# Optimization experiments

Measured on AMD Instinct MI355X. Metric: run time of the kernel, lower is better.

Reference implementation:

```python
import jax, jax.numpy as jnp
import numpy as np

NUM_HEADS = 8
NUM_LEVELS = 4
NUM_POINTS = 16
NUM_BEV = 2
EMBED = 256
BS = 64
NQ = NUM_LEVELS * NUM_POINTS  # 64


def _bilinear_sample(img, grid):
    """F.grid_sample(mode='bilinear', padding_mode='zeros', align_corners=False).
    img: (N, C, H, W); grid: (N, Hg, Wg, 2) in [-1, 1] (x, y). Returns (N, C, Hg, Wg)."""
    N, C, H, W = img.shape
    gx = (grid[..., 0] + 1.0) * (W * 0.5) - 0.5  # (N, Hg, Wg)
    gy = (grid[..., 1] + 1.0) * (H * 0.5) - 0.5
    x0 = jnp.floor(gx)
    y0 = jnp.floor(gy)
    flat = img.reshape(N, C, H * W)

    def gather(xi, yi):
        valid = (xi >= 0) & (xi <= W - 1) & (yi >= 0) & (yi <= H - 1)
        xc = jnp.clip(xi, 0, W - 1).astype(jnp.int32)
        yc = jnp.clip(yi, 0, H - 1).astype(jnp.int32)
        idx = (yc * W + xc).reshape(N, 1, -1)
        g = jnp.take_along_axis(flat, idx, axis=2).reshape(N, C, xi.shape[1], xi.shape[2])
        return g * valid[:, None, :, :].astype(img.dtype)

    wx1 = (gx - x0)[:, None]  # (N,1,Hg,Wg)
    wy1 = (gy - y0)[:, None]
    v00 = gather(x0, y0)
    v01 = gather(x0 + 1.0, y0)
    v10 = gather(x0, y0 + 1.0)
    v11 = gather(x0 + 1.0, y0 + 1.0)
    top = v00 * (1.0 - wx1) + v01 * wx1
    bot = v10 * (1.0 - wx1) + v11 * wx1
    return top * (1.0 - wy1) + bot * wy1


def _forward(query, key_hist, value_hist, reference_points, W_off, b_off, spatial_shapes):
    bs, nq, d = query.shape
    Hn, L, P, BEV = NUM_HEADS, NUM_LEVELS, NUM_POINTS, NUM_BEV
    dh = d // Hn
    Pb = P * BEV
    ss = np.asarray(spatial_shapes)  # (L, 2) static (h, w)

    queries = jnp.concatenate([query, query], axis=1)           # (bs, 2*nq, d)
    keies = jnp.concatenate([query, key_hist], axis=1)
    values = jnp.concatenate([query, value_hist], axis=1)
    qb = queries.shape[1]

    # sampling offsets projection (the only used learned linear in the original forward)
    off = (queries @ W_off + b_off).reshape(bs, qb, Hn, Pb, L, 2)

    # NOTE: original re-assigns q/k/v from the RAW concatenated tensors (to_Q/to_K/to_V discarded)
    qh = queries.reshape(bs, qb, Hn, dh)
    kh = keies.reshape(bs, qb, Hn, dh)
    vh = values.reshape(bs, qb, Hn, dh)

    attn = jax.nn.softmax(jnp.einsum('bqhd,bkhd->bqhk', qh, kh), axis=-1)
    attn = attn.reshape(bs, qb, Hn, L, Pb)

    rp = jnp.concatenate([reference_points, reference_points], axis=1)  # (bs, qb, L, 2)
    norm = jnp.stack([jnp.asarray(ss[:, 1], jnp.float32),
                      jnp.asarray(ss[:, 0], jnp.float32)], axis=-1)      # (L, 2) = (w, h)
    loc = rp[:, :, None, None, :, :] + off / norm                        # (bs,qb,H,Pb,L,2)
    # FAITHFUL: original uses .view here (pure reshape, not a transpose)
    loc = loc.reshape(bs, qb, Hn, L, Pb, 2)
    grids = 2.0 * loc - 1.0

    sampled = []
    start = 0
    for l in range(L):
        h_, w_ = int(ss[l, 0]), int(ss[l, 1])
        vl = vh[:, start:start + h_ * w_]                                # (bs, hw, H, dh)
        start += h_ * w_
        img = vl.transpose(0, 2, 3, 1).reshape(bs * Hn, dh, h_, w_)      # (bs*H, dh, h, w)
        grid_l = grids[:, :, :, l].transpose(0, 2, 1, 3, 4).reshape(bs * Hn, qb, Pb, 2)
        sampled.append(_bilinear_sample(img, grid_l))                    # (bs*H, dh, qb, Pb)

    samp = jnp.stack(sampled, axis=-2).reshape(bs * Hn, dh, qb, L * Pb)
    aw = attn.transpose(0, 2, 1, 3, 4).reshape(bs * Hn, 1, qb, L * Pb)
    out = (samp * aw).sum(-1)                                            # (bs*H, dh, qb)
    # FAITHFUL: original reshapes q_bev dim as (nq, BEV) and means over BEV
    out = out.reshape(bs, Hn * dh, nq, BEV).mean(-1).transpose(0, 2, 1)  # (bs, nq, d)
    return out + query  # dropout is identity at eval


def setup_inputs() -> dict:
    key = jax.random.key(0)
    ks = jax.random.split(key, 6)
    query = jax.random.normal(ks[0], (BS, NQ, EMBED), jnp.float32)
    key_hist = jax.random.normal(ks[1], (BS, NQ, EMBED), jnp.float32)
    value_hist = jax.random.normal(ks[2], (BS, NQ, EMBED), jnp.float32)
    reference_points = jax.random.uniform(ks[3], (BS, NQ, NUM_LEVELS, 2), jnp.float32)
    spatial_shapes = jnp.array([[4, 8]] * NUM_LEVELS, dtype=jnp.int32)  # sum(h*w)=128=L*P*BEV
    off_dim = NUM_HEADS * NUM_BEV * NUM_POINTS * NUM_LEVELS * 2
    W_off = jax.random.normal(ks[4], (EMBED, off_dim), jnp.float32) * 0.02
    b_off = jnp.zeros((off_dim,), jnp.float32)
    return {"query": query, "key_hist": key_hist, "value_hist": value_hist,
            "reference_points": reference_points, "spatial_shapes": spatial_shapes,
            "W_off": W_off, "b_off": b_off}


def reference(query, key_hist, value_hist, reference_points, spatial_shapes, W_off, b_off):
    return _forward(query, key_hist, value_hist, reference_points, W_off, b_off, spatial_shapes)
```

## Files before the change

kernel.cpp:

```cpp
#include <hip/hip_runtime.h>


typedef short  s16x8 __attribute__((ext_vector_type(8)));
typedef short  s16x4 __attribute__((ext_vector_type(4)));
typedef float  f32x4 __attribute__((ext_vector_type(4)));

__device__ __forceinline__ unsigned short f2bf(float f) {
    union { float f; unsigned u; } v; v.f = f;
    unsigned r = v.u + 0x7FFFu + ((v.u >> 16) & 1u);
    return (unsigned short)(r >> 16);
}
__device__ __forceinline__ float bf2f(unsigned short u) {
    return __uint_as_float(((unsigned)u) << 16);
}

__global__ __launch_bounds__(256) void prep(
    const float* __restrict__ W, const float* __restrict__ query,
    const float* __restrict__ key_hist,
    short* __restrict__ Wtb, short* __restrict__ Qb, short* __restrict__ Khb)
{
    __shared__ float s[32][33];
    const int bx = blockIdx.x, t = threadIdx.x;
    if (bx < 512) {
        const int n0 = (bx & 63) * 32, k0 = (bx >> 6) * 32;
        const int c = t & 31, r0 = t >> 5;
        #pragma unroll
        for (int p = 0; p < 4; ++p) {
            const int r = r0 + p * 8;
            s[r][c] = W[(size_t)(k0 + r) * 2048 + n0 + c];
        }
        __syncthreads();
        #pragma unroll
        for (int p = 0; p < 4; ++p) {
            const int r = r0 + p * 8;
            Wtb[(size_t)(n0 + r) * 256 + k0 + c] = (short)f2bf(s[c][r]);
        }
    } else {
        const int j = bx - 512;
        const bool isK = j >= 1024;
        const float* src = isK ? key_hist : query;
        short* dst = isK ? Khb : Qb;
        const int i4 = ((j & 1023) * 256 + t) * 4;
        const float4 v = *(const float4*)(src + i4);
        s16x4 o;
        o.x = (short)f2bf(v.x); o.y = (short)f2bf(v.y);
        o.z = (short)f2bf(v.z); o.w = (short)f2bf(v.w);
        *(s16x4*)(dst + i4) = o;
    }
}

__global__ __launch_bounds__(256, 2) void mega4(
    const float* __restrict__ query, const float* __restrict__ value_hist,
    const float* __restrict__ refp,
    const short* __restrict__ Qb, const short* __restrict__ Khb,
    const short* __restrict__ Wtb, const float* __restrict__ bias,
    float* __restrict__ out)
{
    const int h = blockIdx.x, b = blockIdx.y;
    const int t = threadIdx.x, lane = t & 63, wave = t >> 6;
    const int quad = lane >> 4, col = lane & 15;
    const int wq = wave * 16;

    __shared__ __align__(16) short VTl[32 * 136];
    __shared__ __align__(16) short attLb[64 * 136];
    __shared__ __align__(16) float rpsL[512];
    __shared__ __align__(16) float Am[64 * 132];
    __shared__ __align__(16) short Amb[64 * 136];

    {
        const int p = t >> 1, hf = (t & 1) * 16;
        const float* src = ((p < 64) ? query : value_hist) +
                           (size_t)(b * 64 + (p & 63)) * 256 + h * 32 + hf;
        #pragma unroll
        for (int u = 0; u < 4; ++u) {
            const float4 v = *(const float4*)(src + 4 * u);
            VTl[(hf + 4 * u + 0) * 136 + p] = (short)f2bf(v.x);
            VTl[(hf + 4 * u + 1) * 136 + p] = (short)f2bf(v.y);
            VTl[(hf + 4 * u + 2) * 136 + p] = (short)f2bf(v.z);
            VTl[(hf + 4 * u + 3) * 136 + p] = (short)f2bf(v.w);
        }
    }
    rpsL[t]       = refp[(size_t)b * 512 + t];
    rpsL[t + 256] = refp[(size_t)b * 512 + t + 256];
    #pragma unroll
    for (int u = 0; u < 33; ++u) Am[t + 256 * u] = 0.f;

    f32x4 acc[4][4] = {};
    #pragma unroll
    for (int kq = 0; kq < 4; ++kq) {
        s16x8 afp[4][2], bfp[4][2];
        #pragma unroll
        for (int mi = 0; mi < 4; ++mi)
            #pragma unroll
            for (int ks = 0; ks < 2; ++ks)
                afp[mi][ks] = *(const s16x8*)(Qb +
                    ((size_t)b * 64 + 16 * mi + col) * 256
                    + kq * 64 + ks * 32 + quad * 8);
        #pragma unroll
        for (int nj = 0; nj < 4; ++nj)
            #pragma unroll
            for (int ks = 0; ks < 2; ++ks)
                bfp[nj][ks] = *(const s16x8*)(Wtb +
                    ((size_t)(h * 256 + wave * 64 + 16 * nj + col)) * 256
                    + kq * 64 + ks * 32 + quad * 8);
        #pragma unroll
        for (int ks = 0; ks < 2; ++ks)
            #pragma unroll
            for (int mi = 0; mi < 4; ++mi)
                #pragma unroll
                for (int nj = 0; nj < 4; ++nj)
                    acc[mi][nj] = __builtin_amdgcn_mfma_f32_16x16x32_bf16(
                        afp[mi][ks], bfp[nj][ks], acc[mi][nj], 0, 0, 0);
    }

    {
        const s16x8 aq = *(const s16x8*)(Qb +
            ((size_t)b * 64 + wq + col) * 256 + h * 32 + quad * 8);
        f32x4 lacc[8];
        #pragma unroll
        for (int t8 = 0; t8 < 8; ++t8) {
            const short* src = (t8 < 4)
                ? (Qb  + ((size_t)b * 64 + 16 * t8 + col) * 256)
                : (Khb + ((size_t)b * 64 + 16 * (t8 - 4) + col) * 256);
            const s16x8 bk = *(const s16x8*)(src + h * 32 + quad * 8);
            const f32x4 z = {0.f, 0.f, 0.f, 0.f};
            lacc[t8] = __builtin_amdgcn_mfma_f32_16x16x32_bf16(aq, bk, z, 0, 0, 0);
        }
        #pragma unroll
        for (int r = 0; r < 4; ++r) {
            float m = lacc[0][r];
            #pragma unroll
            for (int t8 = 1; t8 < 8; ++t8) m = fmaxf(m, lacc[t8][r]);
            #pragma unroll
            for (int s = 1; s < 16; s <<= 1) m = fmaxf(m, __shfl_xor(m, s, 64));
            float e[8], ssum = 0.f;
            #pragma unroll
            for (int t8 = 0; t8 < 8; ++t8) {
                e[t8] = __expf(lacc[t8][r] - m); ssum += e[t8];
            }
            #pragma unroll
            for (int s = 1; s < 16; s <<= 1) ssum += __shfl_xor(ssum, s, 64);
            const float inv = 1.0f / ssum;
            const int q = wq + 4 * quad + r;
            #pragma unroll
            for (int t8 = 0; t8 < 8; ++t8)
                attLb[q * 136 + 16 * t8 + col] = (short)f2bf(e[t8] * inv);
        }
    }

    float bjv[4];
    #pragma unroll
    for (int nj = 0; nj < 4; ++nj)
        bjv[nj] = bias[h * 256 + wave * 64 + 16 * nj + col];

    __syncthreads();

    {
        const int i   = col >> 1;
        const int par = col & 1;
        const int base = 32 * wave;
        #pragma unroll
        for (int nj = 0; nj < 4; ++nj) {
            const int f = 32 * wave + 8 * nj + i;
            #pragma unroll
            for (int mi = 0; mi < 4; ++mi) {
                float v[4], p[4];
                #pragma unroll
                for (int r = 0; r < 4; ++r) v[r] = acc[mi][nj][r] + bjv[nj];
                #pragma unroll
                for (int r = 0; r < 4; ++r) p[r] = __shfl_xor(v[r], 1, 64);
                #pragma unroll
                for (int rs = 0; rs < 2; ++rs) {
                    const int r = par * 2 + rs;
                    const float ox = par ? p[r] : v[r];
                    const float oy = par ? v[r] : p[r];
                    const int q = 16 * mi + 4 * quad + r;
                    const float2 rp = *(const float2*)&rpsL[q * 8 + (i & 3) * 2];
                    const float a = bf2f((unsigned short)attLb[q * 136 + f]);
                    const float gx = 8.f * (rp.x + ox * 0.125f) - 0.5f;
                    const float gy = 4.f * (rp.y + oy * 0.25f) - 0.5f;
                    const float x0f = floorf(gx), y0f = floorf(gy);
                    const float wx = gx - x0f, wy = gy - y0f;
                    const int x0 = (int)x0f, y0 = (int)y0f;
                    float* rowW = &Am[q * 132 + base];
                    const bool xv0 = (x0 >= 0) && (x0 < 8);
                    const bool xv1 = (x0 >= -1) && (x0 < 7);
                    const bool yv0 = (y0 >= 0) && (y0 < 4);
                    const bool yv1 = (y0 >= -1) && (y0 < 3);
                    if (xv0 && yv0) unsafeAtomicAdd(&rowW[y0 * 8 + x0],           a * (1.f - wx) * (1.f - wy));
                    if (xv1 && yv0) unsafeAtomicAdd(&rowW[y0 * 8 + x0 + 1],       a * wx * (1.f - wy));
                    if (xv0 && yv1) unsafeAtomicAdd(&rowW[(y0 + 1) * 8 + x0],     a * (1.f - wx) * wy);
                    if (xv1 && yv1) unsafeAtomicAdd(&rowW[(y0 + 1) * 8 + x0 + 1], a * wx * wy);
                }
            }
        }
    }
    __syncthreads();

    {
        const int cq = t >> 2, cc = (t & 3) * 32;
        #pragma unroll
        for (int u = 0; u < 4; ++u) {
            const f32x4 v0 = *(const f32x4*)&Am[cq * 132 + cc + 8 * u];
            const f32x4 v1 = *(const f32x4*)&Am[cq * 132 + cc + 8 * u + 4];
            s16x8 o;
            o[0] = (short)f2bf(v0[0]); o[1] = (short)f2bf(v0[1]);
            o[2] = (short)f2bf(v0[2]); o[3] = (short)f2bf(v0[3]);
            o[4] = (short)f2bf(v1[0]); o[5] = (short)f2bf(v1[1]);
            o[6] = (short)f2bf(v1[2]); o[7] = (short)f2bf(v1[3]);
            *(s16x8*)&Amb[cq * 136 + cc + u * 8] = o;
        }
    }
    __syncthreads();

    {
        f32x4 oacc[2] = {};
        #pragma unroll
        for (int ks = 0; ks < 4; ++ks) {
            const s16x8 af = *(const s16x8*)&Amb[(wq + col) * 136 + ks * 32 + quad * 8];
            #pragma unroll
            for (int n2 = 0; n2 < 2; ++n2) {
                const s16x8 bv = *(const s16x8*)&VTl[(n2 * 16 + col) * 136
                                                     + ks * 32 + quad * 8];
                oacc[n2] = __builtin_amdgcn_mfma_f32_16x16x32_bf16(af, bv, oacc[n2], 0, 0, 0);
            }
        }
        #pragma unroll
        for (int n2 = 0; n2 < 2; ++n2) {
            const int d = h * 32 + n2 * 16 + col;
            #pragma unroll
            for (int pr = 0; pr < 2; ++pr) {
                const float avg = 0.5f * (oacc[n2][2 * pr] + oacc[n2][2 * pr + 1]);
                const int pj = wave * 8 + quad * 2 + pr;
                const size_t re = ((size_t)b * 64 + pj) * 256 + d;
                const size_t ro = ((size_t)b * 64 + pj + 32) * 256 + d;
                out[re] = query[re] + avg;
                out[ro] = query[ro] + avg;
            }
        }
    }
}

extern "C" void kernel_launch(void* const* d_in, const int* in_sizes, int n_in,
                              void* d_out, int out_size, void* d_ws, size_t ws_size,
                              hipStream_t stream) {
    (void)in_sizes; (void)n_in; (void)out_size; (void)ws_size;
    const float* query      = (const float*)d_in[0];
    const float* key_hist   = (const float*)d_in[1];
    const float* value_hist = (const float*)d_in[2];
    const float* refp       = (const float*)d_in[3];
    const float* W_off      = (const float*)d_in[5];
    const float* b_off      = (const float*)d_in[6];

    char* ws = (char*)d_ws;
    short* Wtb = (short*)(ws);
    short* Qb  = (short*)(ws + (1u << 20));
    short* Khb = (short*)(ws + (3u << 20));
    float* out = (float*)d_out;

    prep<<<2560, 256, 0, stream>>>(W_off, query, key_hist, Wtb, Qb, Khb);
    mega4<<<dim3(8, 64), 256, 0, stream>>>(query, value_hist, refp,
                                           Qb, Khb, Wtb, b_off, out);
}
```

Baseline: 165.7 us.

## Split each batch-head block across two query halves to double grid parallelism

The fused kernel now launches 1024 blocks instead of 512, with each block handling 32 of the 64 queries for a (batch, head) pair. Shared memory per block shrinks because the Amb buffer is aliased onto attLb, and launch bounds rise to allow 4 blocks per CU, aiming for better occupancy and more blocks in flight on the GPU. The cost is redundant work: each half still converts the full V tile, reloads the offset-projection weights, and runs the softmax on only two waves, so some waves sit idle.

```diff
diff --git a/kernel.cpp b/kernel.cpp
--- a/kernel.cpp
+++ b/kernel.cpp
@@ -49,23 +49,22 @@
     }
 }
 
-__global__ __launch_bounds__(256, 2) void mega4(
+__global__ __launch_bounds__(256, 4) void mega5(
     const float* __restrict__ query, const float* __restrict__ value_hist,
     const float* __restrict__ refp,
     const short* __restrict__ Qb, const short* __restrict__ Khb,
     const short* __restrict__ Wtb, const float* __restrict__ bias,
     float* __restrict__ out)
 {
-    const int h = blockIdx.x, b = blockIdx.y;
+    const int b = blockIdx.x, h = blockIdx.y, qh = blockIdx.z;
     const int t = threadIdx.x, lane = t & 63, wave = t >> 6;
     const int quad = lane >> 4, col = lane & 15;
-    const int wq = wave * 16;
+    const int qbase = 32 * qh;
 
     __shared__ __align__(16) short VTl[32 * 136];
-    __shared__ __align__(16) short attLb[64 * 136];
-    __shared__ __align__(16) float rpsL[512];
-    __shared__ __align__(16) float Am[64 * 132];
-    __shared__ __align__(16) short Amb[64 * 136];
+    __shared__ __align__(16) short attLb[32 * 136];
+    __shared__ __align__(16) float rpsL[256];
+    __shared__ __align__(16) float Am[32 * 132];
 
     {
         const int p = t >> 1, hf = (t & 1) * 16;
@@ -80,21 +79,21 @@
             VTl[(hf + 4 * u + 3) * 136 + p] = (short)f2bf(v.w);
         }
     }
-    rpsL[t]       = refp[(size_t)b * 512 + t];
-    rpsL[t + 256] = refp[(size_t)b * 512 + t + 256];
+    rpsL[t & 255] = refp[(size_t)b * 512 + qbase * 8 + (t & 255)];
     #pragma unroll
-    for (int u = 0; u < 33; ++u) Am[t + 256 * u] = 0.f;
-
-    f32x4 acc[4][4] = {};
+    for (int u = 0; u < 16; ++u) Am[t + 256 * u] = 0.f;
+    if (t < 128) Am[4096 + t] = 0.f;
+
+    f32x4 acc[2][4] = {};
     #pragma unroll
     for (int kq = 0; kq < 4; ++kq) {
-        s16x8 afp[4][2], bfp[4][2];
-        #pragma unroll
-        for (int mi = 0; mi < 4; ++mi)
+        s16x8 afp[2][2], bfp[4][2];
+        #pragma unroll
+        for (int mi = 0; mi < 2; ++mi)
             #pragma unroll
             for (int ks = 0; ks < 2; ++ks)
                 afp[mi][ks] = *(const s16x8*)(Qb +
-                    ((size_t)b * 64 + 16 * mi + col) * 256
+                    ((size_t)b * 64 + qbase + 16 * mi + col) * 256
                     + kq * 64 + ks * 32 + quad * 8);
         #pragma unroll
         for (int nj = 0; nj < 4; ++nj)
@@ -106,16 +105,17 @@
         #pragma unroll
         for (int ks = 0; ks < 2; ++ks)
             #pragma unroll
-            for (int mi = 0; mi < 4; ++mi)
+            for (int mi = 0; mi < 2; ++mi)
                 #pragma unroll
                 for (int nj = 0; nj < 4; ++nj)
                     acc[mi][nj] = __builtin_amdgcn_mfma_f32_16x16x32_bf16(
                         afp[mi][ks], bfp[nj][ks], acc[mi][nj], 0, 0, 0);
     }
 
-    {
+    if (wave < 2) {
+        const int s = wave;
         const s16x8 aq = *(const s16x8*)(Qb +
-            ((size_t)b * 64 + wq + col) * 256 + h * 32 + quad * 8);
+            ((size_t)b * 64 + qbase + 16 * s + col) * 256 + h * 32 + quad * 8);
         f32x4 lacc[8];
         #pragma unroll
         for (int t8 = 0; t8 < 8; ++t8) {
@@ -132,19 +132,19 @@
             #pragma unroll
             for (int t8 = 1; t8 < 8; ++t8) m = fmaxf(m, lacc[t8][r]);
             #pragma unroll
-            for (int s = 1; s < 16; s <<= 1) m = fmaxf(m, __shfl_xor(m, s, 64));
+            for (int sh = 1; sh < 16; sh <<= 1) m = fmaxf(m, __shfl_xor(m, sh, 64));
             float e[8], ssum = 0.f;
             #pragma unroll
             for (int t8 = 0; t8 < 8; ++t8) {
                 e[t8] = __expf(lacc[t8][r] - m); ssum += e[t8];
             }
             #pragma unroll
-            for (int s = 1; s < 16; s <<= 1) ssum += __shfl_xor(ssum, s, 64);
+            for (int sh = 1; sh < 16; sh <<= 1) ssum += __shfl_xor(ssum, sh, 64);
             const float inv = 1.0f / ssum;
-            const int q = wq + 4 * quad + r;
+            const int ql = 16 * s + 4 * quad + r;
             #pragma unroll
             for (int t8 = 0; t8 < 8; ++t8)
-                attLb[q * 136 + 16 * t8 + col] = (short)f2bf(e[t8] * inv);
+                attLb[ql * 136 + 16 * t8 + col] = (short)f2bf(e[t8] * inv);
         }
     }
 
@@ -163,7 +163,7 @@
         for (int nj = 0; nj < 4; ++nj) {
             const int f = 32 * wave + 8 * nj + i;
             #pragma unroll
-            for (int mi = 0; mi < 4; ++mi) {
+            for (int mi = 0; mi < 2; ++mi) {
                 float v[4], p[4];
                 #pragma unroll
                 for (int r = 0; r < 4; ++r) v[r] = acc[mi][nj][r] + bjv[nj];
@@ -174,15 +174,15 @@
                     const int r = par * 2 + rs;
                     const float ox = par ? p[r] : v[r];
                     const float oy = par ? v[r] : p[r];
-                    const int q = 16 * mi + 4 * quad + r;
-                    const float2 rp = *(const float2*)&rpsL[q * 8 + (i & 3) * 2];
-                    const float a = bf2f((unsigned short)attLb[q * 136 + f]);
+                    const int ql = 16 * mi + 4 * quad + r;
+                    const float2 rp = *(const float2*)&rpsL[ql * 8 + (i & 3) * 2];
+                    const float a = bf2f((unsigned short)attLb[ql * 136 + f]);
                     const float gx = 8.f * (rp.x + ox * 0.125f) - 0.5f;
                     const float gy = 4.f * (rp.y + oy * 0.25f) - 0.5f;
                     const float x0f = floorf(gx), y0f = floorf(gy);
                     const float wx = gx - x0f, wy = gy - y0f;
                     const int x0 = (int)x0f, y0 = (int)y0f;
-                    float* rowW = &Am[q * 132 + base];
+                    float* rowW = &Am[ql * 132 + base];
                     const bool xv0 = (x0 >= 0) && (x0 < 8);
                     const bool xv1 = (x0 >= -1) && (x0 < 7);
                     const bool yv0 = (y0 >= 0) && (y0 < 4);
@@ -198,9 +198,10 @@
     __syncthreads();
 
     {
-        const int cq = t >> 2, cc = (t & 3) * 32;
-        #pragma unroll
-        for (int u = 0; u < 4; ++u) {
+        short* Amb = attLb;
+        const int cq = t >> 3, cc = (t & 7) * 16;
+        #pragma unroll
+        for (int u = 0; u < 2; ++u) {
             const f32x4 v0 = *(const f32x4*)&Am[cq * 132 + cc + 8 * u];
             const f32x4 v1 = *(const f32x4*)&Am[cq * 132 + cc + 8 * u + 4];
             s16x8 o;
@@ -214,29 +215,26 @@
     __syncthreads();
 
     {
-        f32x4 oacc[2] = {};
+        const short* Amb = attLb;
+        const int s = wave & 1, n2 = wave >> 1;
+        f32x4 oacc = {0.f, 0.f, 0.f, 0.f};
         #pragma unroll
         for (int ks = 0; ks < 4; ++ks) {
-            const s16x8 af = *(const s16x8*)&Amb[(wq + col) * 136 + ks * 32 + quad * 8];
-            #pragma unroll
-            for (int n2 = 0; n2 < 2; ++n2) {
-                const s16x8 bv = *(const s16x8*)&VTl[(n2 * 16 + col) * 136
-                                                     + ks * 32 + quad * 8];
-                oacc[n2] = __builtin_amdgcn_mfma_f32_16x16x32_bf16(af, bv, oacc[n2], 0, 0, 0);
-            }
-        }
-        #pragma unroll
-        for (int n2 = 0; n2 < 2; ++n2) {
-            const int d = h * 32 + n2 * 16 + col;
-            #pragma unroll
-            for (int pr = 0; pr < 2; ++pr) {
-                const float avg = 0.5f * (oacc[n2][2 * pr] + oacc[n2][2 * pr + 1]);
-                const int pj = wave * 8 + quad * 2 + pr;
-                const size_t re = ((size_t)b * 64 + pj) * 256 + d;
-                const size_t ro = ((size_t)b * 64 + pj + 32) * 256 + d;
-                out[re] = query[re] + avg;
-                out[ro] = query[ro] + avg;
-            }
+            const s16x8 af = *(const s16x8*)&Amb[(16 * s + col) * 136
+                                                 + ks * 32 + quad * 8];
+            const s16x8 bv = *(const s16x8*)&VTl[(n2 * 16 + col) * 136
+                                                 + ks * 32 + quad * 8];
+            oacc = __builtin_amdgcn_mfma_f32_16x16x32_bf16(af, bv, oacc, 0, 0, 0);
+        }
+        const int d = h * 32 + n2 * 16 + col;
+        #pragma unroll
+        for (int pr = 0; pr < 2; ++pr) {
+            const float avg = 0.5f * (oacc[2 * pr] + oacc[2 * pr + 1]);
+            const int pj = qh * 16 + s * 8 + quad * 2 + pr;
+            const size_t re = ((size_t)b * 64 + pj) * 256 + d;
+            const size_t ro = ((size_t)b * 64 + pj + 32) * 256 + d;
+            out[re] = query[re] + avg;
+            out[ro] = query[ro] + avg;
         }
     }
 }
@@ -259,6 +257,6 @@
     float* out = (float*)d_out;
 
     prep<<<2560, 256, 0, stream>>>(W_off, query, key_hist, Wtb, Qb, Khb);
-    mega4<<<dim3(8, 64), 256, 0, stream>>>(query, value_hist, refp,
-                                           Qb, Khb, Wtb, b_off, out);
-}
+    mega5<<<dim3(64, 8, 2), 256, 0, stream>>>(query, value_hist, refp,
+                                              Qb, Khb, Wtb, b_off, out);
+}
```

After: 171.1 us. 1.03x slower.

## Fuse bf16 conversion prep kernel into main kernel, loading fp32 directly

Applied to the files above, without the earlier changes.

Removes the separate prep kernel that transposed W_off and converted query and key_hist to bf16 in workspace. The main kernel now loads fp32 data and converts it to bf16 in registers, reading W columns with strided scalar loads. The grid is reordered so batch is the fast dimension and blocks sharing the same head's W slice run together for cache reuse. This saves a launch and a workspace round trip, but the W loads are uncoalesced, with eight strided scalar loads per fragment, and every block repeats the conversion work.

```diff
diff --git a/kernel.cpp b/kernel.cpp
--- a/kernel.cpp
+++ b/kernel.cpp
@@ -2,7 +2,6 @@
 
 
 typedef short  s16x8 __attribute__((ext_vector_type(8)));
-typedef short  s16x4 __attribute__((ext_vector_type(4)));
 typedef float  f32x4 __attribute__((ext_vector_type(4)));
 
 __device__ __forceinline__ unsigned short f2bf(float f) {
@@ -13,50 +12,32 @@
 __device__ __forceinline__ float bf2f(unsigned short u) {
     return __uint_as_float(((unsigned)u) << 16);
 }
-
-__global__ __launch_bounds__(256) void prep(
-    const float* __restrict__ W, const float* __restrict__ query,
-    const float* __restrict__ key_hist,
-    short* __restrict__ Wtb, short* __restrict__ Qb, short* __restrict__ Khb)
-{
-    __shared__ float s[32][33];
-    const int bx = blockIdx.x, t = threadIdx.x;
-    if (bx < 512) {
-        const int n0 = (bx & 63) * 32, k0 = (bx >> 6) * 32;
-        const int c = t & 31, r0 = t >> 5;
-        #pragma unroll
-        for (int p = 0; p < 4; ++p) {
-            const int r = r0 + p * 8;
-            s[r][c] = W[(size_t)(k0 + r) * 2048 + n0 + c];
-        }
-        __syncthreads();
-        #pragma unroll
-        for (int p = 0; p < 4; ++p) {
-            const int r = r0 + p * 8;
-            Wtb[(size_t)(n0 + r) * 256 + k0 + c] = (short)f2bf(s[c][r]);
-        }
-    } else {
-        const int j = bx - 512;
-        const bool isK = j >= 1024;
-        const float* src = isK ? key_hist : query;
-        short* dst = isK ? Khb : Qb;
-        const int i4 = ((j & 1023) * 256 + t) * 4;
-        const float4 v = *(const float4*)(src + i4);
-        s16x4 o;
-        o.x = (short)f2bf(v.x); o.y = (short)f2bf(v.y);
-        o.z = (short)f2bf(v.z); o.w = (short)f2bf(v.w);
-        *(s16x4*)(dst + i4) = o;
-    }
-}
-
-__global__ __launch_bounds__(256, 2) void mega4(
-    const float* __restrict__ query, const float* __restrict__ value_hist,
-    const float* __restrict__ refp,
-    const short* __restrict__ Qb, const short* __restrict__ Khb,
-    const short* __restrict__ Wtb, const float* __restrict__ bias,
+__device__ __forceinline__ s16x8 ld8bf(const float* __restrict__ p) {
+    const float4 v0 = *(const float4*)p;
+    const float4 v1 = *(const float4*)(p + 4);
+    s16x8 o;
+    o[0] = (short)f2bf(v0.x); o[1] = (short)f2bf(v0.y);
+    o[2] = (short)f2bf(v0.z); o[3] = (short)f2bf(v0.w);
+    o[4] = (short)f2bf(v1.x); o[5] = (short)f2bf(v1.y);
+    o[6] = (short)f2bf(v1.z); o[7] = (short)f2bf(v1.w);
+    return o;
+}
+__device__ __forceinline__ s16x8 ldcol8bf(const float* __restrict__ W,
+                                          int k, int n) {
+    s16x8 o;
+    #pragma unroll
+    for (int j = 0; j < 8; ++j)
+        o[j] = (short)f2bf(W[(size_t)(k + j) * 2048 + n]);
+    return o;
+}
+
+__global__ __launch_bounds__(256, 2) void mega6(
+    const float* __restrict__ query, const float* __restrict__ key_hist,
+    const float* __restrict__ value_hist, const float* __restrict__ refp,
+    const float* __restrict__ W, const float* __restrict__ bias,
     float* __restrict__ out)
 {
-    const int h = blockIdx.x, b = blockIdx.y;
+    const int b = blockIdx.x, h = blockIdx.y;
     const int t = threadIdx.x, lane = t & 63, wave = t >> 6;
     const int quad = lane >> 4, col = lane & 15;
     const int wq = wave * 16;
@@ -93,16 +74,16 @@
         for (int mi = 0; mi < 4; ++mi)
             #pragma unroll
             for (int ks = 0; ks < 2; ++ks)
-                afp[mi][ks] = *(const s16x8*)(Qb +
+                afp[mi][ks] = ld8bf(query +
                     ((size_t)b * 64 + 16 * mi + col) * 256
                     + kq * 64 + ks * 32 + quad * 8);
         #pragma unroll
         for (int nj = 0; nj < 4; ++nj)
             #pragma unroll
             for (int ks = 0; ks < 2; ++ks)
-                bfp[nj][ks] = *(const s16x8*)(Wtb +
-                    ((size_t)(h * 256 + wave * 64 + 16 * nj + col)) * 256
-                    + kq * 64 + ks * 32 + quad * 8);
+                bfp[nj][ks] = ldcol8bf(W,
+                    kq * 64 + ks * 32 + quad * 8,
+                    h * 256 + wave * 64 + 16 * nj + col);
         #pragma unroll
         for (int ks = 0; ks < 2; ++ks)
             #pragma unroll
@@ -114,15 +95,15 @@
     }
 
     {
-        const s16x8 aq = *(const s16x8*)(Qb +
+        const s16x8 aq = ld8bf(query +
             ((size_t)b * 64 + wq + col) * 256 + h * 32 + quad * 8);
         f32x4 lacc[8];
         #pragma unroll
         for (int t8 = 0; t8 < 8; ++t8) {
-            const short* src = (t8 < 4)
-                ? (Qb  + ((size_t)b * 64 + 16 * t8 + col) * 256)
-                : (Khb + ((size_t)b * 64 + 16 * (t8 - 4) + col) * 256);
-            const s16x8 bk = *(const s16x8*)(src + h * 32 + quad * 8);
+            const float* src = (t8 < 4)
+                ? (query    + ((size_t)b * 64 + 16 * t8 + col) * 256)
+                : (key_hist + ((size_t)b * 64 + 16 * (t8 - 4) + col) * 256);
+            const s16x8 bk = ld8bf(src + h * 32 + quad * 8);
             const f32x4 z = {0.f, 0.f, 0.f, 0.f};
             lacc[t8] = __builtin_amdgcn_mfma_f32_16x16x32_bf16(aq, bk, z, 0, 0, 0);
         }
@@ -244,21 +225,15 @@
 extern "C" void kernel_launch(void* const* d_in, const int* in_sizes, int n_in,
                               void* d_out, int out_size, void* d_ws, size_t ws_size,
                               hipStream_t stream) {
-    (void)in_sizes; (void)n_in; (void)out_size; (void)ws_size;
+    (void)in_sizes; (void)n_in; (void)out_size; (void)d_ws; (void)ws_size;
     const float* query      = (const float*)d_in[0];
     const float* key_hist   = (const float*)d_in[1];
     const float* value_hist = (const float*)d_in[2];
     const float* refp       = (const float*)d_in[3];
     const float* W_off      = (const float*)d_in[5];
     const float* b_off      = (const float*)d_in[6];
-
-    char* ws = (char*)d_ws;
-    short* Wtb = (short*)(ws);
-    short* Qb  = (short*)(ws + (1u << 20));
-    short* Khb = (short*)(ws + (3u << 20));
     float* out = (float*)d_out;
 
-    prep<<<2560, 256, 0, stream>>>(W_off, query, key_hist, Wtb, Qb, Khb);
-    mega4<<<dim3(8, 64), 256, 0, stream>>>(query, value_hist, refp,
-                                           Qb, Khb, Wtb, b_off, out);
-}
+    mega6<<<dim3(64, 8), 256, 0, stream>>>(query, key_hist, value_hist, refp,
+                                           W_off, b_off, out);
+}
```

After: 169.8 us. 1.02x slower.
